# Performance work log

Measured on AMD Instinct MI355X. Metric: run time of the kernel, lower is better.

The kernel has to match this reference:

```python
import jax, jax.numpy as jnp
import numpy as np

B, S, D, H = 2, 2048, 1024, 16
HD = D // H  # head_dim = 64


def setup_inputs() -> dict:
    key = jax.random.key(0)
    ks = jax.random.split(key, 12)
    s = 1.0 / np.sqrt(D)
    return {
        "q": jax.random.normal(ks[0], (B, S, D), jnp.float32),
        "k": jax.random.normal(ks[1], (B, S, D), jnp.float32),
        "v": jax.random.normal(ks[2], (B, S, D), jnp.float32),
        "mask": jnp.zeros((B, 1, 1, S), jnp.float32),
        "wq": jax.random.normal(ks[3], (D, D), jnp.float32) * s,
        "bq": jnp.zeros((D,), jnp.float32),
        "wk": jax.random.normal(ks[4], (D, D), jnp.float32) * s,
        "bk": jnp.zeros((D,), jnp.float32),
        "wv": jax.random.normal(ks[5], (D, D), jnp.float32) * s,
        "bv": jnp.zeros((D,), jnp.float32),
        "wo": jax.random.normal(ks[6], (D, D), jnp.float32) * s,
        "bo": jnp.zeros((D,), jnp.float32),
    }


def _split_heads(x):
    # [B, S, D] -> [B, H, S, HD]
    return x.reshape(B, S, H, HD).transpose(0, 2, 1, 3)


def reference(q, k, v, mask, wq, bq, wk, bk, wv, bv, wo, bo):
    _q = _split_heads(q @ wq + bq)
    _k = _split_heads(k @ wk + bk)
    _v = _split_heads(v @ wv + bv)
    scale = jnp.sqrt(jnp.float32(HD)) + 1e-8
    score = jnp.einsum("bhqd,bhkd->bhqk", _q, _k) / scale
    score = score + mask * -1e9
    attn = jax.nn.softmax(score, axis=-1)
    ctx = jnp.einsum("bhqk,bhkd->bhqd", attn, _v)
    ctx = ctx.transpose(0, 2, 1, 3).reshape(B, S, D)
    # dropout is identity at inference (training=False)
    return ctx @ wo + bo
```

## Files before the change

kernel.cpp:

```cpp
#include <hip/hip_runtime.h>
#include <hip/hip_bf16.h>

typedef unsigned short u16;
typedef __attribute__((ext_vector_type(8))) short s16x8;
typedef __attribute__((ext_vector_type(4))) short s16x4;
typedef __attribute__((ext_vector_type(4))) float f32x4;
typedef __attribute__((ext_vector_type(8))) unsigned short u16x8;
typedef __attribute__((ext_vector_type(4))) unsigned int u32x4;
typedef __attribute__((ext_vector_type(2))) unsigned int u32x2;

#define AS1(p) (const __attribute__((address_space(1))) void*)(p)
#define AS3(p) (__attribute__((address_space(3))) void*)(p)

__device__ __forceinline__ u16 f2bf(float f) {
  unsigned u = __builtin_bit_cast(unsigned, f);
  u += 0x7fffu + ((u >> 16) & 1u);
  return (u16)(u >> 16);
}

__device__ __forceinline__ unsigned cvtpk(float lo, float hi) {
  unsigned r;
  asm("v_cvt_pk_bf16_f32 %0, %1, %2" : "=v"(r) : "v"(lo), "v"(hi));
  return r;
}

__global__ __launch_bounds__(256) void prep(const float* __restrict__ q,
                                            const float* __restrict__ k,
                                            const float* __restrict__ v,
                                            const float* __restrict__ wq,
                                            const float* __restrict__ wk,
                                            const float* __restrict__ wv,
                                            const float* __restrict__ wo,
                                            u16* __restrict__ Xq, u16* __restrict__ Xk,
                                            u16* __restrict__ Xv, u16* __restrict__ Wqt,
                                            u16* __restrict__ Wkt, u16* __restrict__ Wvt,
                                            u16* __restrict__ Wot) {
  __shared__ float t[32][33];
  const int bid = blockIdx.x, tid = threadIdx.x;
  if (bid < 6144) {
    const int m = bid >> 11;
    const float* in = m == 0 ? q : m == 1 ? k : v;
    u16* out = m == 0 ? Xq : m == 1 ? Xk : Xv;
    const int i = ((bid & 2047) * 256 + tid) * 8;
    f32x4 a = *(const f32x4*)(in + i);
    f32x4 b = *(const f32x4*)(in + i + 4);
    u16x8 r;
    r[0] = f2bf(a[0]); r[1] = f2bf(a[1]); r[2] = f2bf(a[2]); r[3] = f2bf(a[3]);
    r[4] = f2bf(b[0]); r[5] = f2bf(b[1]); r[6] = f2bf(b[2]); r[7] = f2bf(b[3]);
    *(u16x8*)(out + i) = r;
  } else {
    const int b2 = bid - 6144;
    const int wsel = b2 >> 10;
    const float* w = wsel == 0 ? wq : wsel == 1 ? wk : wsel == 2 ? wv : wo;
    u16* wt = wsel == 0 ? Wqt : wsel == 1 ? Wkt : wsel == 2 ? Wvt : Wot;
    const int n0 = (b2 & 31) * 32, k0 = ((b2 >> 5) & 31) * 32;
    const int tx = tid & 31, ty = tid >> 5;
#pragma unroll
    for (int i = 0; i < 4; i++)
      t[ty + 8 * i][tx] = w[(size_t)(k0 + ty + 8 * i) * 1024 + n0 + tx];
    __syncthreads();
#pragma unroll
    for (int i = 0; i < 4; i++)
      wt[(size_t)(n0 + ty + 8 * i) * 1024 + k0 + tx] = f2bf(t[tx][ty + 8 * i]);
  }
}

__global__ __launch_bounds__(256) void gemm_qkv(const u16* __restrict__ Xq,
                                                const u16* __restrict__ Xk,
                                                const u16* __restrict__ Xv,
                                                const u16* __restrict__ Wqt,
                                                const u16* __restrict__ Wkt,
                                                const u16* __restrict__ Wvt,
                                                const float* __restrict__ bq,
                                                const float* __restrict__ bk,
                                                const float* __restrict__ bv,
                                                u16* __restrict__ Qb, u16* __restrict__ Kb,
                                                u16* __restrict__ Vt) {
  const int mode = blockIdx.z;
  const u16* A = mode == 0 ? Xq : mode == 1 ? Xk : Xv;
  const u16* Bt = mode == 0 ? Wqt : mode == 1 ? Wkt : Wvt;
  const float* bias = mode == 0 ? bq : mode == 1 ? bk : bv;
  u16* outp = mode == 0 ? Qb : mode == 1 ? Kb : Vt;

  __shared__ u16 Als[128 * 64];
  __shared__ u16 Bls[128 * 64];
  const int tid = threadIdx.x;
  const int lane = tid & 63;
  const int wid = tid >> 6;
  const int wm = wid >> 1, wn = wid & 1;
  const int sid = blockIdx.x + (blockIdx.y << 3);
  const int xcd = sid & 7, sj = sid >> 3;
  const int m0 = ((xcd << 2) + (sj & 3)) * 128;
  const int n0 = (sj >> 2) * 128;
  const int g = lane >> 4, c = lane & 15;
  const int srl = lane >> 3, sch0 = lane & 7;
  f32x4 acc[4][4] = {};
  for (int kk = 0; kk < 1024; kk += 64) {
    __syncthreads();
#pragma unroll
    for (int jj = 0; jj < 4; jj++) {
      const int rl = wid * 32 + jj * 8 + srl;
      const int col = kk + ((sch0 ^ (rl & 7)) << 3);
      __builtin_amdgcn_global_load_lds(AS1(A + (size_t)(m0 + rl) * 1024 + col),
                                       AS3(&Als[(wid * 32 + jj * 8) * 64]), 16, 0, 0);
      __builtin_amdgcn_global_load_lds(AS1(Bt + (size_t)(n0 + rl) * 1024 + col),
                                       AS3(&Bls[(wid * 32 + jj * 8) * 64]), 16, 0, 0);
    }
    __syncthreads();
#pragma unroll
    for (int half = 0; half < 2; half++) {
      s16x8 af[4], bfr[4];
#pragma unroll
      for (int mi = 0; mi < 4; mi++) {
        const int r = wm * 64 + mi * 16 + c;
        af[mi] = *(const s16x8*)&Als[r * 64 + (((half * 4 + g) ^ (r & 7)) << 3)];
      }
#pragma unroll
      for (int ni = 0; ni < 4; ni++) {
        const int r = wn * 64 + ni * 16 + c;
        bfr[ni] = *(const s16x8*)&Bls[r * 64 + (((half * 4 + g) ^ (r & 7)) << 3)];
      }
      __builtin_amdgcn_s_setprio(1);
#pragma unroll
      for (int mi = 0; mi < 4; mi++)
#pragma unroll
        for (int ni = 0; ni < 4; ni++)
          acc[mi][ni] = __builtin_amdgcn_mfma_f32_16x16x32_bf16(af[mi], bfr[ni],
                                                                acc[mi][ni], 0, 0, 0);
      __builtin_amdgcn_s_setprio(0);
    }
  }
#pragma unroll
  for (int mi = 0; mi < 4; mi++) {
#pragma unroll
    for (int ni = 0; ni < 4; ni++) {
      const int gn = n0 + wn * 64 + ni * 16 + c;
      const float bb = bias[gn];
      const int gmb = m0 + wm * 64 + mi * 16 + (g << 2);
      const int hd = gn >> 6, d = gn & 63;
      if (mode == 2) {
        const int b = gmb >> 11, s0 = gmb & 2047;
        const int tile = s0 >> 6;
        const int jb = gmb & 63;
        const int j5b = jb & 31;
        const int posb = ((jb >> 5) << 5) + (((j5b & 15) >> 2) << 3) + ((j5b >> 4) << 2);
        s16x4 st;
#pragma unroll
        for (int r = 0; r < 4; r++) st[r] = (short)f2bf(acc[mi][ni][r] + bb);
        *(s16x4*)&Vt[(((size_t)b * 16 + hd) * 64 + d) * 2048 + tile * 64 + posb] = st;
      } else {
#pragma unroll
        for (int r = 0; r < 4; r++) {
          const int gm = gmb + r;
          float val = acc[mi][ni][r] + bb;
          const int b = gm >> 11, s = gm & 2047;
          if (mode == 0) val *= 0.18033688f;
          outp[(((size_t)b * 16 + hd) * 2048 + s) * 64 + d] = f2bf(val);
        }
      }
    }
  }
}

__global__ __launch_bounds__(256) void gemm_out(const u16* __restrict__ A,
                                                const u16* __restrict__ Bt,
                                                const float* __restrict__ bias,
                                                float* __restrict__ outp) {
  __shared__ u16 Als[128 * 64];
  __shared__ u16 Bls[64 * 64];
  const int tid = threadIdx.x;
  const int lane = tid & 63;
  const int wid = tid >> 6;
  const int sid = blockIdx.x + (blockIdx.y << 4);
  const int xcd = sid & 7, sj = sid >> 3;
  const int m0 = ((xcd << 2) + (sj & 3)) * 128;
  const int n0 = (sj >> 2) * 64;
  const int g = lane >> 4, c = lane & 15;
  const int srl = lane >> 3, sch0 = lane & 7;
  f32x4 acc[2][4] = {};
  for (int kk = 0; kk < 1024; kk += 64) {
    __syncthreads();
#pragma unroll
    for (int jj = 0; jj < 4; jj++) {
      const int rl = wid * 32 + jj * 8 + srl;
      const int col = kk + ((sch0 ^ (rl & 7)) << 3);
      __builtin_amdgcn_global_load_lds(AS1(A + (size_t)(m0 + rl) * 1024 + col),
                                       AS3(&Als[(wid * 32 + jj * 8) * 64]), 16, 0, 0);
    }
#pragma unroll
    for (int jj = 0; jj < 2; jj++) {
      const int rl = wid * 16 + jj * 8 + srl;
      const int col = kk + ((sch0 ^ (rl & 7)) << 3);
      __builtin_amdgcn_global_load_lds(AS1(Bt + (size_t)(n0 + rl) * 1024 + col),
                                       AS3(&Bls[(wid * 16 + jj * 8) * 64]), 16, 0, 0);
    }
    __syncthreads();
#pragma unroll
    for (int half = 0; half < 2; half++) {
      s16x8 af[2], bfr[4];
#pragma unroll
      for (int mi = 0; mi < 2; mi++) {
        const int r = wid * 32 + mi * 16 + c;
        af[mi] = *(const s16x8*)&Als[r * 64 + (((half * 4 + g) ^ (r & 7)) << 3)];
      }
#pragma unroll
      for (int ni = 0; ni < 4; ni++) {
        const int r = ni * 16 + c;
        bfr[ni] = *(const s16x8*)&Bls[r * 64 + (((half * 4 + g) ^ (r & 7)) << 3)];
      }
      __builtin_amdgcn_s_setprio(1);
#pragma unroll
      for (int mi = 0; mi < 2; mi++)
#pragma unroll
        for (int ni = 0; ni < 4; ni++)
          acc[mi][ni] = __builtin_amdgcn_mfma_f32_16x16x32_bf16(af[mi], bfr[ni],
                                                                acc[mi][ni], 0, 0, 0);
      __builtin_amdgcn_s_setprio(0);
    }
  }
#pragma unroll
  for (int mi = 0; mi < 2; mi++) {
#pragma unroll
    for (int ni = 0; ni < 4; ni++) {
      const int gn = n0 + ni * 16 + c;
      const float bb = bias[gn];
      const int gmb = m0 + wid * 32 + mi * 16 + (g << 2);
#pragma unroll
      for (int r = 0; r < 4; r++)
        outp[(size_t)(gmb + r) * 1024 + gn] = acc[mi][ni][r] + bb;
    }
  }
}

__global__ __launch_bounds__(128) void attn_fwd(const u16* __restrict__ Qb,
                                                const u16* __restrict__ Kb,
                                                const u16* __restrict__ Vt,
                                                const float* __restrict__ mask,
                                                u16* __restrict__ ctx) {
  __shared__ u16 Kls[2][4096];
  __shared__ u16 Vls[2][4096];
  const int tid = threadIdx.x;
  const int lane = tid & 63, wid = tid >> 6;
  const int n = blockIdx.x;
  const int bh = ((n & 7) << 2) | ((n >> 3) & 3);
  const int qblk = n >> 5;
  const int b = bh >> 4, hd = bh & 15;
  const int g = lane >> 4, c = lane & 15;
  const int qbase = qblk * 64 + wid * 32;

  const float* mp = mask + (size_t)b * 2048;
  int th_any = 0;
#pragma unroll
  for (int i = 0; i < 8; i++) {
    const f32x4 m4 = *(const f32x4*)(mp + lane * 32 + i * 4);
    th_any |= (m4[0] != 0.f) | (m4[1] != 0.f) | (m4[2] != 0.f) | (m4[3] != 0.f);
  }
  const int havemask = (__ballot(th_any) != 0ULL);

  s16x8 qf[2][2];
#pragma unroll
  for (int sub = 0; sub < 2; sub++) {
    const u16* Qp = Qb + ((size_t)bh * 2048 + qbase + sub * 16 + c) * 64;
    qf[sub][0] = *(const s16x8*)(Qp + g * 8);
    qf[sub][1] = *(const s16x8*)(Qp + 32 + g * 8);
  }

  const u16* Kbh = Kb + (size_t)bh * 2048 * 64;
  const u16* Vbh = Vt + (size_t)bh * 64 * 2048;

  const int srl = lane >> 3;
  const int sch0 = lane & 7;
  auto STAGE = [&](int kv0, int bufi) {
#pragma unroll
    for (int jj = 0; jj < 4; jj++) {
      const int rl = wid * 32 + jj * 8 + srl;
      const int sch = sch0 ^ (rl & 7);
      __builtin_amdgcn_global_load_lds(AS1(Kbh + (size_t)(kv0 + rl) * 64 + sch * 8),
                                       AS3(&Kls[bufi][wid * 2048 + jj * 512]), 16, 0, 0);
      __builtin_amdgcn_global_load_lds(AS1(Vbh + (size_t)rl * 2048 + kv0 + sch * 8),
                                       AS3(&Vls[bufi][wid * 2048 + jj * 512]), 16, 0, 0);
    }
  };

  f32x4 o[2][4] = {};
  f32x4 ts2[2] = {};

  STAGE(0, 0);
  STAGE(64, 1);

  for (int t = 0; t < 32; t++) {
    const int kv0 = t * 64;
    const int buf = t & 1;
    if (t < 31) {
      asm volatile("s_waitcnt vmcnt(8)" ::: "memory");
    } else {
      asm volatile("s_waitcnt vmcnt(0)" ::: "memory");
    }
    __builtin_amdgcn_sched_barrier(0);
    __builtin_amdgcn_s_barrier();
    __builtin_amdgcn_sched_barrier(0);

    f32x4 sacc[2][4] = {};
#pragma unroll
    for (int kvt = 0; kvt < 4; kvt++) {
      const int row = kvt * 16 + c;
      const int s7 = row & 7;
      const s16x8 kf0 = *(const s16x8*)&Kls[buf][row * 64 + ((g ^ s7) << 3)];
      const s16x8 kf1 = *(const s16x8*)&Kls[buf][row * 64 + (((4 + g) ^ s7) << 3)];
      sacc[0][kvt] = __builtin_amdgcn_mfma_f32_16x16x32_bf16(kf0, qf[0][0], sacc[0][kvt], 0, 0, 0);
      sacc[0][kvt] = __builtin_amdgcn_mfma_f32_16x16x32_bf16(kf1, qf[0][1], sacc[0][kvt], 0, 0, 0);
      sacc[1][kvt] = __builtin_amdgcn_mfma_f32_16x16x32_bf16(kf0, qf[1][0], sacc[1][kvt], 0, 0, 0);
      sacc[1][kvt] = __builtin_amdgcn_mfma_f32_16x16x32_bf16(kf1, qf[1][1], sacc[1][kvt], 0, 0, 0);
    }

    s16x8 vreg[4][2];
#pragma unroll
    for (int dblk = 0; dblk < 4; dblk++) {
      const int row = dblk * 16 + c;
      const int s7 = row & 7;
      const u16* base = &Vls[buf][row * 64];
      vreg[dblk][0] = *(const s16x8*)(base + ((g ^ s7) << 3));
      vreg[dblk][1] = *(const s16x8*)(base + (((4 + g) ^ s7) << 3));
    }
    asm volatile("s_waitcnt lgkmcnt(0)" ::: "memory");
    __builtin_amdgcn_sched_barrier(0);
    __builtin_amdgcn_s_barrier();
    __builtin_amdgcn_sched_barrier(0);
    if (t < 30) STAGE(kv0 + 128, buf);

    s16x8 pf[2][2];
    if (!havemask) {
#pragma unroll
      for (int qs = 0; qs < 2; qs++) {
        f32x4 p4[4];
#pragma unroll
        for (int kvt = 0; kvt < 4; kvt++) {
#pragma unroll
          for (int jj = 0; jj < 4; jj++)
            p4[kvt][jj] = __builtin_amdgcn_exp2f(sacc[qs][kvt][jj]);
          ts2[qs] += p4[kvt];
        }
#pragma unroll
        for (int sub = 0; sub < 2; sub++) {
          u32x4 ww;
          ww[0] = cvtpk(p4[sub * 2][0], p4[sub * 2][1]);
          ww[1] = cvtpk(p4[sub * 2][2], p4[sub * 2][3]);
          ww[2] = cvtpk(p4[sub * 2 + 1][0], p4[sub * 2 + 1][1]);
          ww[3] = cvtpk(p4[sub * 2 + 1][2], p4[sub * 2 + 1][3]);
          pf[qs][sub] = __builtin_bit_cast(s16x8, ww);
        }
      }
    } else {
      f32x4 mk[4];
#pragma unroll
      for (int kvt = 0; kvt < 4; kvt++)
        mk[kvt] = *(const f32x4*)(mp + kv0 + kvt * 16 + 4 * g);
#pragma unroll
      for (int qs = 0; qs < 2; qs++) {
        f32x4 p4[4];
#pragma unroll
        for (int kvt = 0; kvt < 4; kvt++) {
#pragma unroll
          for (int jj = 0; jj < 4; jj++)
            p4[kvt][jj] = __builtin_amdgcn_exp2f(fmaf(mk[kvt][jj], -1.44269504e9f,
                                                      sacc[qs][kvt][jj]));
          ts2[qs] += p4[kvt];
        }
#pragma unroll
        for (int sub = 0; sub < 2; sub++) {
          u32x4 ww;
          ww[0] = cvtpk(p4[sub * 2][0], p4[sub * 2][1]);
          ww[1] = cvtpk(p4[sub * 2][2], p4[sub * 2][3]);
          ww[2] = cvtpk(p4[sub * 2 + 1][0], p4[sub * 2 + 1][1]);
          ww[3] = cvtpk(p4[sub * 2 + 1][2], p4[sub * 2 + 1][3]);
          pf[qs][sub] = __builtin_bit_cast(s16x8, ww);
        }
      }
    }

#pragma unroll
    for (int dblk = 0; dblk < 4; dblk++)
#pragma unroll
      for (int subk = 0; subk < 2; subk++) {
        o[0][dblk] = __builtin_amdgcn_mfma_f32_16x16x32_bf16(vreg[dblk][subk], pf[0][subk], o[0][dblk], 0, 0, 0);
        o[1][dblk] = __builtin_amdgcn_mfma_f32_16x16x32_bf16(vreg[dblk][subk], pf[1][subk], o[1][dblk], 0, 0, 0);
      }
  }

#pragma unroll
  for (int qs = 0; qs < 2; qs++) {
    float ts = (ts2[qs][0] + ts2[qs][1]) + (ts2[qs][2] + ts2[qs][3]);
    ts += __shfl_xor(ts, 16);
    ts += __shfl_xor(ts, 32);
    const float inv = 1.0f / ts;
    u16* cp = ctx + ((size_t)b * 2048 + qbase + qs * 16 + c) * 1024 + hd * 64;
#pragma unroll
    for (int d = 0; d < 4; d++) {
      u32x2 st;
      st[0] = cvtpk(o[qs][d][0] * inv, o[qs][d][1] * inv);
      st[1] = cvtpk(o[qs][d][2] * inv, o[qs][d][3] * inv);
      *(u32x2*)&cp[d * 16 + 4 * g] = st;
    }
  }
}

extern "C" void kernel_launch(void* const* d_in, const int* in_sizes, int n_in,
                              void* d_out, int out_size, void* d_ws, size_t ws_size,
                              hipStream_t stream) {
  (void)in_sizes; (void)n_in; (void)out_size; (void)ws_size;
  const float* q = (const float*)d_in[0];
  const float* k = (const float*)d_in[1];
  const float* v = (const float*)d_in[2];
  const float* mask = (const float*)d_in[3];
  const float* wq = (const float*)d_in[4];
  const float* bq = (const float*)d_in[5];
  const float* wk = (const float*)d_in[6];
  const float* bk = (const float*)d_in[7];
  const float* wv = (const float*)d_in[8];
  const float* bv = (const float*)d_in[9];
  const float* wo = (const float*)d_in[10];
  const float* bo = (const float*)d_in[11];
  float* out = (float*)d_out;
  char* ws = (char*)d_ws;
  const size_t MB = (size_t)1 << 20;
  u16* Xq = (u16*)(ws + 0 * MB);
  u16* Xk = (u16*)(ws + 8 * MB);
  u16* Xv = (u16*)(ws + 16 * MB);
  u16* Wqt = (u16*)(ws + 24 * MB);
  u16* Wkt = (u16*)(ws + 26 * MB);
  u16* Wvt = (u16*)(ws + 28 * MB);
  u16* Wot = (u16*)(ws + 30 * MB);
  u16* Qb = (u16*)(ws + 32 * MB);
  u16* Kb = (u16*)(ws + 40 * MB);
  u16* Vt = (u16*)(ws + 48 * MB);
  u16* ctx = Xq;

  prep<<<10240, 256, 0, stream>>>(q, k, v, wq, wk, wv, wo, Xq, Xk, Xv, Wqt, Wkt, Wvt, Wot);
  gemm_qkv<<<dim3(8, 32, 3), 256, 0, stream>>>(Xq, Xk, Xv, Wqt, Wkt, Wvt, bq, bk, bv,
                                               Qb, Kb, Vt);
  attn_fwd<<<1024, 128, 0, stream>>>(Qb, Kb, Vt, mask, ctx);
  gemm_out<<<dim3(16, 32), 256, 0, stream>>>(ctx, Wot, bo, out);
}
```

Measured before the change: 126.8 us.

## Double-buffer LDS tiles in projection GEMMs with async prefetch

Both the QKV projection GEMM and the output projection GEMM now use two LDS buffers of 32-wide K tiles instead of one 64-wide tile. The global-to-LDS load for step t+2 is issued right after the fragments are read, using explicit vmcnt waits and barriers, so it overlaps with the MFMA work. The intent is to hide global load latency that the old load-sync-compute loop exposed. In exchange there are twice as many loop iterations and barriers per K sweep, and correctness now depends on the hand-counted vmcnt values.

```diff
diff --git a/kernel.cpp b/kernel.cpp
--- a/kernel.cpp
+++ b/kernel.cpp
@@ -82,8 +82,8 @@
   const float* bias = mode == 0 ? bq : mode == 1 ? bk : bv;
   u16* outp = mode == 0 ? Qb : mode == 1 ? Kb : Vt;
 
-  __shared__ u16 Als[128 * 64];
-  __shared__ u16 Bls[128 * 64];
+  __shared__ u16 Als[2][128 * 32];
+  __shared__ u16 Bls[2][128 * 32];
   const int tid = threadIdx.x;
   const int lane = tid & 63;
   const int wid = tid >> 6;
@@ -93,42 +93,57 @@
   const int m0 = ((xcd << 2) + (sj & 3)) * 128;
   const int n0 = (sj >> 2) * 128;
   const int g = lane >> 4, c = lane & 15;
-  const int srl = lane >> 3, sch0 = lane & 7;
+  const int srow = lane >> 2, schunk = lane & 3;
+
+  auto STAGE = [&](int kk, int bufi) {
+#pragma unroll
+    for (int i = 0; i < 2; i++) {
+      const int row = i * 64 + wid * 16 + srow;
+      const int col = kk + ((schunk ^ (row & 3)) << 3);
+      __builtin_amdgcn_global_load_lds(AS1(A + (size_t)(m0 + row) * 1024 + col),
+                                       AS3(&Als[bufi][(i * 64 + wid * 16) * 32]), 16, 0, 0);
+      __builtin_amdgcn_global_load_lds(AS1(Bt + (size_t)(n0 + row) * 1024 + col),
+                                       AS3(&Bls[bufi][(i * 64 + wid * 16) * 32]), 16, 0, 0);
+    }
+  };
+
   f32x4 acc[4][4] = {};
-  for (int kk = 0; kk < 1024; kk += 64) {
-    __syncthreads();
-#pragma unroll
-    for (int jj = 0; jj < 4; jj++) {
-      const int rl = wid * 32 + jj * 8 + srl;
-      const int col = kk + ((sch0 ^ (rl & 7)) << 3);
-      __builtin_amdgcn_global_load_lds(AS1(A + (size_t)(m0 + rl) * 1024 + col),
-                                       AS3(&Als[(wid * 32 + jj * 8) * 64]), 16, 0, 0);
-      __builtin_amdgcn_global_load_lds(AS1(Bt + (size_t)(n0 + rl) * 1024 + col),
-                                       AS3(&Bls[(wid * 32 + jj * 8) * 64]), 16, 0, 0);
-    }
-    __syncthreads();
-#pragma unroll
-    for (int half = 0; half < 2; half++) {
-      s16x8 af[4], bfr[4];
-#pragma unroll
-      for (int mi = 0; mi < 4; mi++) {
-        const int r = wm * 64 + mi * 16 + c;
-        af[mi] = *(const s16x8*)&Als[r * 64 + (((half * 4 + g) ^ (r & 7)) << 3)];
-      }
-#pragma unroll
-      for (int ni = 0; ni < 4; ni++) {
-        const int r = wn * 64 + ni * 16 + c;
-        bfr[ni] = *(const s16x8*)&Bls[r * 64 + (((half * 4 + g) ^ (r & 7)) << 3)];
-      }
-      __builtin_amdgcn_s_setprio(1);
-#pragma unroll
-      for (int mi = 0; mi < 4; mi++)
-#pragma unroll
-        for (int ni = 0; ni < 4; ni++)
-          acc[mi][ni] = __builtin_amdgcn_mfma_f32_16x16x32_bf16(af[mi], bfr[ni],
-                                                                acc[mi][ni], 0, 0, 0);
-      __builtin_amdgcn_s_setprio(0);
-    }
+  STAGE(0, 0);
+  STAGE(32, 1);
+  for (int t = 0; t < 32; t++) {
+    const int buf = t & 1;
+    if (t < 31) {
+      asm volatile("s_waitcnt vmcnt(4)" ::: "memory");
+    } else {
+      asm volatile("s_waitcnt vmcnt(0)" ::: "memory");
+    }
+    __builtin_amdgcn_sched_barrier(0);
+    __builtin_amdgcn_s_barrier();
+    __builtin_amdgcn_sched_barrier(0);
+    s16x8 af[4], bfr[4];
+#pragma unroll
+    for (int mi = 0; mi < 4; mi++) {
+      const int r = wm * 64 + mi * 16 + c;
+      af[mi] = *(const s16x8*)&Als[buf][r * 32 + ((g ^ (r & 3)) << 3)];
+    }
+#pragma unroll
+    for (int ni = 0; ni < 4; ni++) {
+      const int r = wn * 64 + ni * 16 + c;
+      bfr[ni] = *(const s16x8*)&Bls[buf][r * 32 + ((g ^ (r & 3)) << 3)];
+    }
+    asm volatile("s_waitcnt lgkmcnt(0)" ::: "memory");
+    __builtin_amdgcn_sched_barrier(0);
+    __builtin_amdgcn_s_barrier();
+    __builtin_amdgcn_sched_barrier(0);
+    if (t < 30) STAGE((t + 2) * 32, buf);
+    __builtin_amdgcn_s_setprio(1);
+#pragma unroll
+    for (int mi = 0; mi < 4; mi++)
+#pragma unroll
+      for (int ni = 0; ni < 4; ni++)
+        acc[mi][ni] = __builtin_amdgcn_mfma_f32_16x16x32_bf16(af[mi], bfr[ni],
+                                                              acc[mi][ni], 0, 0, 0);
+    __builtin_amdgcn_s_setprio(0);
   }
 #pragma unroll
   for (int mi = 0; mi < 4; mi++) {
@@ -166,8 +181,8 @@
                                                 const u16* __restrict__ Bt,
                                                 const float* __restrict__ bias,
                                                 float* __restrict__ outp) {
-  __shared__ u16 Als[128 * 64];
-  __shared__ u16 Bls[64 * 64];
+  __shared__ u16 Als[2][128 * 32];
+  __shared__ u16 Bls[2][64 * 32];
   const int tid = threadIdx.x;
   const int lane = tid & 63;
   const int wid = tid >> 6;
@@ -176,47 +191,61 @@
   const int m0 = ((xcd << 2) + (sj & 3)) * 128;
   const int n0 = (sj >> 2) * 64;
   const int g = lane >> 4, c = lane & 15;
-  const int srl = lane >> 3, sch0 = lane & 7;
+  const int srow = lane >> 2, schunk = lane & 3;
+
+  auto STAGE = [&](int kk, int bufi) {
+#pragma unroll
+    for (int i = 0; i < 2; i++) {
+      const int row = i * 64 + wid * 16 + srow;
+      const int col = kk + ((schunk ^ (row & 3)) << 3);
+      __builtin_amdgcn_global_load_lds(AS1(A + (size_t)(m0 + row) * 1024 + col),
+                                       AS3(&Als[bufi][(i * 64 + wid * 16) * 32]), 16, 0, 0);
+    }
+    {
+      const int row = wid * 16 + srow;
+      const int col = kk + ((schunk ^ (row & 3)) << 3);
+      __builtin_amdgcn_global_load_lds(AS1(Bt + (size_t)(n0 + row) * 1024 + col),
+                                       AS3(&Bls[bufi][(wid * 16) * 32]), 16, 0, 0);
+    }
+  };
+
   f32x4 acc[2][4] = {};
-  for (int kk = 0; kk < 1024; kk += 64) {
-    __syncthreads();
-#pragma unroll
-    for (int jj = 0; jj < 4; jj++) {
-      const int rl = wid * 32 + jj * 8 + srl;
-      const int col = kk + ((sch0 ^ (rl & 7)) << 3);
-      __builtin_amdgcn_global_load_lds(AS1(A + (size_t)(m0 + rl) * 1024 + col),
-                                       AS3(&Als[(wid * 32 + jj * 8) * 64]), 16, 0, 0);
-    }
-#pragma unroll
-    for (int jj = 0; jj < 2; jj++) {
-      const int rl = wid * 16 + jj * 8 + srl;
-      const int col = kk + ((sch0 ^ (rl & 7)) << 3);
-      __builtin_amdgcn_global_load_lds(AS1(Bt + (size_t)(n0 + rl) * 1024 + col),
-                                       AS3(&Bls[(wid * 16 + jj * 8) * 64]), 16, 0, 0);
-    }
-    __syncthreads();
-#pragma unroll
-    for (int half = 0; half < 2; half++) {
-      s16x8 af[2], bfr[4];
-#pragma unroll
-      for (int mi = 0; mi < 2; mi++) {
-        const int r = wid * 32 + mi * 16 + c;
-        af[mi] = *(const s16x8*)&Als[r * 64 + (((half * 4 + g) ^ (r & 7)) << 3)];
-      }
-#pragma unroll
-      for (int ni = 0; ni < 4; ni++) {
-        const int r = ni * 16 + c;
-        bfr[ni] = *(const s16x8*)&Bls[r * 64 + (((half * 4 + g) ^ (r & 7)) << 3)];
-      }
-      __builtin_amdgcn_s_setprio(1);
-#pragma unroll
-      for (int mi = 0; mi < 2; mi++)
-#pragma unroll
-        for (int ni = 0; ni < 4; ni++)
-          acc[mi][ni] = __builtin_amdgcn_mfma_f32_16x16x32_bf16(af[mi], bfr[ni],
-                                                                acc[mi][ni], 0, 0, 0);
-      __builtin_amdgcn_s_setprio(0);
-    }
+  STAGE(0, 0);
+  STAGE(32, 1);
+  for (int t = 0; t < 32; t++) {
+    const int buf = t & 1;
+    if (t < 31) {
+      asm volatile("s_waitcnt vmcnt(3)" ::: "memory");
+    } else {
+      asm volatile("s_waitcnt vmcnt(0)" ::: "memory");
+    }
+    __builtin_amdgcn_sched_barrier(0);
+    __builtin_amdgcn_s_barrier();
+    __builtin_amdgcn_sched_barrier(0);
+    s16x8 af[2], bfr[4];
+#pragma unroll
+    for (int mi = 0; mi < 2; mi++) {
+      const int r = wid * 32 + mi * 16 + c;
+      af[mi] = *(const s16x8*)&Als[buf][r * 32 + ((g ^ (r & 3)) << 3)];
+    }
+#pragma unroll
+    for (int ni = 0; ni < 4; ni++) {
+      const int r = ni * 16 + c;
+      bfr[ni] = *(const s16x8*)&Bls[buf][r * 32 + ((g ^ (r & 3)) << 3)];
+    }
+    asm volatile("s_waitcnt lgkmcnt(0)" ::: "memory");
+    __builtin_amdgcn_sched_barrier(0);
+    __builtin_amdgcn_s_barrier();
+    __builtin_amdgcn_sched_barrier(0);
+    if (t < 30) STAGE((t + 2) * 32, buf);
+    __builtin_amdgcn_s_setprio(1);
+#pragma unroll
+    for (int mi = 0; mi < 2; mi++)
+#pragma unroll
+      for (int ni = 0; ni < 4; ni++)
+        acc[mi][ni] = __builtin_amdgcn_mfma_f32_16x16x32_bf16(af[mi], bfr[ni],
+                                                              acc[mi][ni], 0, 0, 0);
+    __builtin_amdgcn_s_setprio(0);
   }
 #pragma unroll
   for (int mi = 0; mi < 2; mi++) {
```

Measured after the change: 120.8 us. 4.7% less time.
